# Optimization experiments

Hardware: AMD Instinct MI355X
Metric: run time of the kernel (lower is better)

## Reference

```python
import jax, jax.numpy as jnp
import numpy as np

N = 20000      # nodes
E = 320000     # edges (avg degree 16)
F_IN = 32      # raw node feature dim
D = 128        # GNN_EMBEDDING_DIM = out_channels per head
HEADS = 4
RNN_H = 128    # RNN_HIDDEN_DIM
NEG_SLOPE = 0.2


def setup_inputs() -> dict:
    key = jax.random.key(0)
    ks = jax.random.split(key, 16)
    s = 0.05
    return {
        "node_features": jax.random.normal(ks[0], (N, F_IN), jnp.float32),
        "hidden_state": jax.random.normal(ks[1], (1, RNN_H), jnp.float32),
        "W_enc": jax.random.normal(ks[2], (F_IN, D), jnp.float32) * s,
        "b_enc": jax.random.normal(ks[3], (D,), jnp.float32) * s,
        "W_l": jax.random.normal(ks[4], (D, HEADS * D), jnp.float32) * s,
        "b_l": jax.random.normal(ks[5], (HEADS * D,), jnp.float32) * s,
        "W_r": jax.random.normal(ks[6], (D, HEADS * D), jnp.float32) * s,
        "b_r": jax.random.normal(ks[7], (HEADS * D,), jnp.float32) * s,
        "att": jax.random.normal(ks[8], (HEADS, D), jnp.float32) * s,
        "gat_bias": jax.random.normal(ks[9], (D,), jnp.float32) * s,
        "W_ih": jax.random.normal(ks[10], (3 * RNN_H, D), jnp.float32) * s,
        "W_hh": jax.random.normal(ks[11], (3 * RNN_H, RNN_H), jnp.float32) * s,
        "b_ih": jax.random.normal(ks[12], (3 * RNN_H,), jnp.float32) * s,
        "b_hh": jax.random.normal(ks[13], (3 * RNN_H,), jnp.float32) * s,
        "edge_index": jax.random.randint(ks[14], (2, E), 0, N, jnp.int32),
    }


def reference(node_features, hidden_state, W_enc, b_enc, W_l, b_l, W_r, b_r,
              att, gat_bias, W_ih, W_hh, b_ih, b_hh, edge_index):
    n = node_features.shape[0]
    # node encoder + ReLU
    h = jax.nn.relu(node_features @ W_enc + b_enc)                 # [N, D]

    # GATv2Conv (heads=4, concat=False), add_self_loops=True, eval (no dropout)
    loop = jnp.arange(n, dtype=edge_index.dtype)
    src = jnp.concatenate([edge_index[0], loop])                   # source j
    dst = jnp.concatenate([edge_index[1], loop])                   # target i

    xl = (h @ W_l + b_l).reshape(n, HEADS, D)                      # source proj
    xr = (h @ W_r + b_r).reshape(n, HEADS, D)                      # target proj

    e = jax.nn.leaky_relu(xl[src] + xr[dst], NEG_SLOPE)            # [Et, H, C]
    logits = jnp.einsum('ehc,hc->eh', e, att)                      # [Et, H]

    # segment softmax over incoming edges of each target node
    m = jax.ops.segment_max(logits, dst, num_segments=n)           # [N, H]
    m = jnp.where(jnp.isfinite(m), m, 0.0)
    p = jnp.exp(logits - m[dst])
    denom = jax.ops.segment_sum(p, dst, num_segments=n)
    alpha = p / jnp.maximum(denom[dst], 1e-16)                     # [Et, H]

    out = jax.ops.segment_sum(xl[src] * alpha[..., None], dst, num_segments=n)
    gat = out.mean(axis=1) + gat_bias                              # [N, D]

    # agent node 0 -> GRUCell (torch gate order: r, z, n)
    x = gat[0:1]                                                   # [1, D]
    gi = x @ W_ih.T + b_ih
    gh = hidden_state @ W_hh.T + b_hh
    i_r, i_z, i_n = jnp.split(gi, 3, axis=-1)
    h_r, h_z, h_n = jnp.split(gh, 3, axis=-1)
    r = jax.nn.sigmoid(i_r + h_r)
    z = jax.nn.sigmoid(i_z + h_z)
    ng = jnp.tanh(i_n + r * h_n)
    return (1.0 - z) * ng + z * hidden_state                       # [1, RNN_H]
```

## Files before the change

kernel.cpp:

```cpp
#include <hip/hip_runtime.h>


#define NXL2 32
#define NSC  96
#define NBLK (NXL2 + NSC)
#define SLOTS 8
#define CAP  40
#define FLAGMAGIC 0x5A5A0000u

#define WEo  0
#define WLo  4096
#define WRo  6144
#define WIo  8192
#define WHo  9728
#define NFo  11264
#define HSo  12544
#define XL2o 17664
#define LGLo 18304
#define ALPo 19584
#define BUFSZ 19744

#define A_LG  0
#define A_XRP 64
#define A_XR  128
#define A_HP  160
#define A_GB  288
#define A_GAT 416
#define A_GH  544
#define A_GI  556
#define A_BI  568
#define A_BH  580

struct KP {
    const int* ei; int E;
    const float *nf, *W_enc, *b_enc, *W_l, *b_l, *W_r, *b_r, *att, *gat_bias,
                *hprev, *W_ih, *W_hh, *b_ih, *b_hh;
    unsigned *scnt;
    unsigned *xlflag;
    unsigned *o0flag;
    int      *sslots;
    float *lgpart;
    float *out0;
    float *out;
};

__device__ __forceinline__ unsigned pollFlag(unsigned* p) {
    for (long it = 0; it < 50000000L; ++it) {
        unsigned v = atomicOr(p, 0u);
        if ((v & 0xFFFF0000u) == FLAGMAGIC) return v & 0xFFFFu;
        __builtin_amdgcn_s_sleep(2);
    }
    return 0u;
}

__device__ __forceinline__ float sigm(float x) { return 1.f / (1.f + expf(-x)); }

__global__ __launch_bounds__(256) void k_all(KP p)
{
    __shared__ __align__(16) float buf[BUFSZ];
    __shared__ float aux[640];
    __shared__ int   iaux[128];
    const int t = threadIdx.x, b = blockIdx.x;

    if (b >= NXL2) {
        int s = b - NXL2;
        if (t == 0) iaux[0] = 0;
        __syncthreads();
        if ((p.E & 3) == 0) {
            int nv = p.E >> 2;
            int per = (nv + NSC - 1) / NSC;
            int lo = s * per, hi = min(lo + per, nv);
            const int4* d4 = (const int4*)(p.ei + p.E);
            for (int base = lo; base < hi; base += 1024) {
                int4 v[4];
                #pragma unroll
                for (int k = 0; k < 4; ++k) {
                    int i = base + t + k * 256;
                    v[k] = (i < hi) ? d4[i] : make_int4(1, 1, 1, 1);
                }
                #pragma unroll
                for (int k = 0; k < 4; ++k) {
                    int i = base + t + k * 256;
                    if (v[k].x == 0 || v[k].y == 0 || v[k].z == 0 || v[k].w == 0) {
                        #pragma unroll
                        for (int c = 0; c < 4; ++c) {
                            if ((&v[k].x)[c] == 0) {
                                int q = atomicAdd(&iaux[0], 1);
                                if (q < SLOTS) iaux[8 + q] = p.ei[4 * (long)i + c];
                            }
                        }
                    }
                }
            }
        } else {
            int per = (p.E + NSC - 1) / NSC;
            long lo = (long)s * per, hi = lo + per; if (hi > p.E) hi = p.E;
            for (long i = lo + t; i < hi; i += 256) {
                if (p.ei[p.E + i] == 0) {
                    int q = atomicAdd(&iaux[0], 1);
                    if (q < SLOTS) iaux[8 + q] = p.ei[i];
                }
            }
        }
        __syncthreads();
        int myc = min(iaux[0], SLOTS);
        if (t < myc) p.sslots[s * SLOTS + t] = iaux[8 + t];
        __syncthreads();
        __threadfence();
        if (t == 0) atomicExch(&p.scnt[s * 16], FLAGMAGIC | (unsigned)myc);
        return;
    }

    const int l4 = t & 15, g16 = t >> 4;
    const int j = b * 16 + l4;

    float blv = p.b_l[j], atv = p.att[j];
    float brv = (t < 16) ? p.b_r[b * 16 + t] : 0.f;
    if (t < 128) { aux[A_HP + t] = p.hprev[t]; aux[A_GB + t] = p.gat_bias[t]; }
    if (t >= 128 && t < 140) {
        int rr = t - 128, gate = rr >> 2, rin = rr & 3;
        aux[A_BI + rr] = p.b_ih[gate * 128 + b * 4 + rin];
        aux[A_BH + rr] = p.b_hh[gate * 128 + b * 4 + rin];
    }

    for (int idx = t; idx < 1024; idx += 256)
        ((float4*)(buf + WEo))[idx] = ((const float4*)p.W_enc)[idx];
    for (int idx = t; idx < 512; idx += 256) {
        int row = idx >> 2, f4 = idx & 3;
        ((float4*)(buf + WLo))[idx] = *(const float4*)(p.W_l + (long)row * 512 + b * 16 + f4 * 4);
    }
    for (int idx = t; idx < 512; idx += 256) {
        int row = idx >> 2, f4 = idx & 3;
        ((float4*)(buf + WRo))[idx] = *(const float4*)(p.W_r + (long)row * 512 + b * 16 + f4 * 4);
    }
    for (int idx = t; idx < 384; idx += 256) {
        int rr = idx >> 5, f4 = idx & 31;
        int grow = (rr >> 2) * 128 + b * 4 + (rr & 3);
        ((float4*)(buf + WIo))[idx] = *(const float4*)(p.W_ih + (long)grow * 128 + f4 * 4);
    }
    for (int idx = t; idx < 384; idx += 256) {
        int rr = idx >> 5, f4 = idx & 31;
        int grow = (rr >> 2) * 128 + b * 4 + (rr & 3);
        ((float4*)(buf + WHo))[idx] = *(const float4*)(p.W_hh + (long)grow * 128 + f4 * 4);
    }

    if (t < NSC) iaux[32 + t] = (int)pollFlag(&p.scnt[t * 16]);
    __syncthreads();
    __threadfence();
    if (t < 64) {
        int s0 = 2 * t, s1 = 2 * t + 1;
        int c0 = (s0 < NSC) ? iaux[32 + s0] : 0;
        int c1 = (s1 < NSC) ? iaux[32 + s1] : 0;
        int sum = c0 + c1, pre = sum;
        #pragma unroll
        for (int off = 1; off < 64; off <<= 1) {
            int v = __shfl_up(pre, off);
            if (t >= off) pre += v;
        }
        int base = pre - sum;
        for (int u = 0; u < c0; ++u) { if (base < CAP - 1) iaux[64 + base] = p.sslots[s0 * SLOTS + u]; ++base; }
        for (int u = 0; u < c1; ++u) { if (base < CAP - 1) iaux[64 + base] = p.sslots[s1 * SLOTS + u]; ++base; }
        if (t == 63) iaux[1] = min(pre, CAP - 1);
    }
    __syncthreads();
    int Mc = iaux[1];
    if (t == 0) iaux[64 + Mc] = 0;
    __syncthreads();
    int Mt = Mc + 1;

    for (int idx = t; idx < Mt * 8; idx += 256) {
        int e = idx >> 3, f4 = idx & 7;
        ((float4*)(buf + NFo))[idx] = *(const float4*)(p.nf + (long)iaux[64 + e] * 32 + f4 * 4);
    }
    __syncthreads();
    {
        int eg = t >> 7, c = t & 127;
        for (int e = eg; e < Mt; e += 2) {
            float a0 = 0, a1 = 0, a2 = 0, a3 = 0;
            #pragma unroll
            for (int k = 0; k < 32; k += 4) {
                a0 += buf[NFo + e * 32 + k]     * buf[WEo + k * 128 + c];
                a1 += buf[NFo + e * 32 + k + 1] * buf[WEo + (k + 1) * 128 + c];
                a2 += buf[NFo + e * 32 + k + 2] * buf[WEo + (k + 2) * 128 + c];
                a3 += buf[NFo + e * 32 + k + 3] * buf[WEo + (k + 3) * 128 + c];
            }
            buf[HSo + e * 128 + c] = fmaxf(a0 + a1 + a2 + a3 + p.b_enc[c], 0.f);
        }
    }
    __syncthreads();
    if (t < 64) {
        int col = t & 15, ch = t >> 4;
        const float* h0 = &buf[HSo + (Mt - 1) * 128];
        float s = 0.f;
        #pragma unroll 8
        for (int cc = 0; cc < 32; ++cc) {
            int c = ch * 32 + cc;
            s += h0[c] * buf[WRo + c * 16 + col];
        }
        aux[A_XRP + t] = s;
    }
    int ne = 0, el[3] = {0, 0, 0};
    for (int e = g16; e < Mt; e += 16) el[ne++] = e;
    float acc[3] = {0, 0, 0};
    #pragma unroll 4
    for (int c = 0; c < 128; c += 4) {
        float w0 = buf[WLo + c * 16 + l4],       w1 = buf[WLo + (c + 1) * 16 + l4];
        float w2 = buf[WLo + (c + 2) * 16 + l4], w3 = buf[WLo + (c + 3) * 16 + l4];
        #pragma unroll
        for (int k = 0; k < 3; ++k) {
            if (k < ne) {
                float4 h4 = *(const float4*)&buf[HSo + el[k] * 128 + c];
                acc[k] += h4.x * w0 + h4.y * w1 + h4.z * w2 + h4.w * w3;
            }
        }
    }
    __syncthreads();
    if (t < 16) aux[A_XR + t] = aux[A_XRP + t] + aux[A_XRP + 16 + t]
                              + aux[A_XRP + 32 + t] + aux[A_XRP + 48 + t] + brv;
    __syncthreads();
    {
        float xrj = aux[A_XR + l4];
        #pragma unroll
        for (int k = 0; k < 3; ++k) {
            if (k < ne) {
                int e = el[k];
                float xv = acc[k] + blv;
                buf[XL2o + e * 16 + l4] = xv;
                float v = xv + xrj;
                v = (v > 0.f) ? v : 0.2f * v;
                float pp = v * atv;
                #pragma unroll
                for (int off = 8; off; off >>= 1) pp += __shfl_down(pp, off, 16);
                if (l4 == 0) aux[A_LG + e] = pp;
            }
        }
    }
    __syncthreads();
    if (t < Mt) p.lgpart[b * CAP + t] = aux[A_LG + t];
    __syncthreads();
    __threadfence();
    if (t == 0) atomicExch(&p.xlflag[b * 16], FLAGMAGIC | 1u);

    {
        int w = t >> 6, l = t & 63;
        #pragma unroll
        for (int i = 0; i < 3; ++i) {
            int rr = w * 3 + i;
            float2 wv = ((const float2*)&buf[WHo + rr * 128])[l];
            float pp = wv.x * aux[A_HP + 2 * l] + wv.y * aux[A_HP + 2 * l + 1];
            #pragma unroll
            for (int off = 32; off; off >>= 1) pp += __shfl_down(pp, off);
            if (l == 0) aux[A_GH + rr] = pp + aux[A_BH + rr];
        }
    }

    if (t < NXL2) pollFlag(&p.xlflag[t * 16]);
    __syncthreads();
    __threadfence();
    for (int idx = t; idx < NXL2 * CAP; idx += 256)
        buf[LGLo + idx] = p.lgpart[idx];
    __syncthreads();
    if (t < 4) {
        int h = t;
        float m = -1e30f;
        for (int e = 0; e < Mt; ++e) {
            float lv = 0.f;
            #pragma unroll
            for (int q = 0; q < 8; ++q) lv += buf[LGLo + (8 * h + q) * CAP + e];
            buf[ALPo + e * 4 + h] = lv;
            m = fmaxf(m, lv);
        }
        float d = 0.f;
        for (int e = 0; e < Mt; ++e) d += expf(buf[ALPo + e * 4 + h] - m);
        float inv = 1.f / fmaxf(d, 1e-16f);
        for (int e = 0; e < Mt; ++e)
            buf[ALPo + e * 4 + h] = expf(buf[ALPo + e * 4 + h] - m) * inv;
    }
    __syncthreads();
    if (t < 16) {
        int h = b >> 3;
        float s = 0.f;
        for (int e = 0; e < Mt; ++e)
            s += buf[ALPo + e * 4 + h] * buf[XL2o + e * 16 + t];
        p.out0[b * 16 + t] = s;
    }
    __syncthreads();
    __threadfence();
    if (t == 0) atomicExch(&p.o0flag[b * 16], FLAGMAGIC | 1u);

    if (t < NXL2) pollFlag(&p.o0flag[t * 16]);
    __syncthreads();
    __threadfence();
    if (t < 128)
        aux[A_GAT + t] = 0.25f * (p.out0[t] + p.out0[128 + t] +
                                  p.out0[256 + t] + p.out0[384 + t]) + aux[A_GB + t];
    __syncthreads();
    {
        int w = t >> 6, l = t & 63;
        #pragma unroll
        for (int i = 0; i < 3; ++i) {
            int rr = w * 3 + i;
            float2 wv = ((const float2*)&buf[WIo + rr * 128])[l];
            float pp = wv.x * aux[A_GAT + 2 * l] + wv.y * aux[A_GAT + 2 * l + 1];
            #pragma unroll
            for (int off = 32; off; off >>= 1) pp += __shfl_down(pp, off);
            if (l == 0) aux[A_GI + rr] = pp + aux[A_BI + rr];
        }
    }
    __syncthreads();
    if (t < 4) {
        int c = b * 4 + t;
        float r = sigm(aux[A_GI + t]     + aux[A_GH + t]);
        float z = sigm(aux[A_GI + 4 + t] + aux[A_GH + 4 + t]);
        float n = tanhf(aux[A_GI + 8 + t] + r * aux[A_GH + 8 + t]);
        p.out[c] = (1.f - z) * n + z * aux[A_HP + c];
    }
}

extern "C" void kernel_launch(void* const* d_in, const int* in_sizes, int n_in,
                              void* d_out, int out_size, void* d_ws, size_t ws_size,
                              hipStream_t stream) {
    KP kp;
    kp.nf       = (const float*)d_in[0];
    kp.hprev    = (const float*)d_in[1];
    kp.W_enc    = (const float*)d_in[2];
    kp.b_enc    = (const float*)d_in[3];
    kp.W_l      = (const float*)d_in[4];
    kp.b_l      = (const float*)d_in[5];
    kp.W_r      = (const float*)d_in[6];
    kp.b_r      = (const float*)d_in[7];
    kp.att      = (const float*)d_in[8];
    kp.gat_bias = (const float*)d_in[9];
    kp.W_ih     = (const float*)d_in[10];
    kp.W_hh     = (const float*)d_in[11];
    kp.b_ih     = (const float*)d_in[12];
    kp.b_hh     = (const float*)d_in[13];
    kp.ei       = (const int*)d_in[14];
    kp.E = in_sizes[14] / 2;

    char* ws = (char*)d_ws;
    kp.scnt   = (unsigned*)(ws + 0);
    kp.xlflag = (unsigned*)(ws + 6144);
    kp.o0flag = (unsigned*)(ws + 8192);
    kp.sslots = (int*)(ws + 10240);
    kp.lgpart = (float*)(ws + 13312);
    kp.out0   = (float*)(ws + 18432);
    kp.out    = (float*)d_out;

    k_all<<<NBLK, 256, 0, stream>>>(kp);
}
```

Before: 118.0 us.

## Move encoder to scanner blocks and drop second grid-wide barrier

Scanner blocks now compute the encoder ReLU output for the source nodes they find and publish those rows, so worker blocks no longer gather raw features and re-encode them after the barrier. The GRU hidden-side matvec, the input-bias-independent gi precompute and the node-0 target projection are moved ahead of the scanner poll, so they overlap the wait. Each worker publishes its full xl slice, and every block then reduces all four heads redundantly, which removes the second flag-based grid barrier (o0flag). The poll loop also drops its sleep, spinning more aggressively, and uses a larger workspace.

```diff
diff --git a/kernel.cpp b/kernel.cpp
--- a/kernel.cpp
+++ b/kernel.cpp
@@ -1,9 +1,9 @@
 #include <hip/hip_runtime.h>
 
 
-#define NXL2 32
-#define NSC  96
-#define NBLK (NXL2 + NSC)
+#define NW   32
+#define NS   96
+#define NBLK (NW + NS)
 #define SLOTS 8
 #define CAP  40
 #define FLAGMAGIC 0x5A5A0000u
@@ -11,25 +11,26 @@
 #define WEo  0
 #define WLo  4096
 #define WRo  6144
-#define WIo  8192
-#define WHo  9728
-#define NFo  11264
-#define HSo  12544
-#define XL2o 17664
-#define LGLo 18304
-#define ALPo 19584
-#define BUFSZ 19744
-
-#define A_LG  0
-#define A_XRP 64
+#define HSo  8192
+#define XLo  0
+#define LGLo 20480
+#define ALPo 21760
+#define WIo  21920
+#define WHo  23456
+#define BUFSZ 24992
+
+#define A_H0  0
 #define A_XR  128
-#define A_HP  160
-#define A_GB  288
-#define A_GAT 416
-#define A_GH  544
-#define A_GI  556
-#define A_BI  568
-#define A_BH  580
+#define A_XRP 144
+#define A_HP  208
+#define A_GH  336
+#define A_GIB 348
+#define A_GAT 360
+#define A_LGP 488
+#define A_NF0 528
+#define A_BI  560
+#define A_BHH 572
+#define AUXSZ 584
 
 struct KP {
     const int* ei; int E;
@@ -37,18 +38,16 @@
                 *hprev, *W_ih, *W_hh, *b_ih, *b_hh;
     unsigned *scnt;
     unsigned *xlflag;
-    unsigned *o0flag;
-    int      *sslots;
+    float *hsslot;
     float *lgpart;
-    float *out0;
+    float *xlpub;
     float *out;
 };
 
 __device__ __forceinline__ unsigned pollFlag(unsigned* p) {
-    for (long it = 0; it < 50000000L; ++it) {
+    for (long it = 0; it < 20000000L; ++it) {
         unsigned v = atomicOr(p, 0u);
         if ((v & 0xFFFF0000u) == FLAGMAGIC) return v & 0xFFFFu;
-        __builtin_amdgcn_s_sleep(2);
     }
     return 0u;
 }
@@ -58,17 +57,17 @@
 __global__ __launch_bounds__(256) void k_all(KP p)
 {
     __shared__ __align__(16) float buf[BUFSZ];
-    __shared__ float aux[640];
-    __shared__ int   iaux[128];
+    __shared__ __align__(16) float aux[AUXSZ];
+    __shared__ int iaux[208];
     const int t = threadIdx.x, b = blockIdx.x;
 
-    if (b >= NXL2) {
-        int s = b - NXL2;
+    if (b >= NW) {
+        int s = b - NW;
         if (t == 0) iaux[0] = 0;
         __syncthreads();
         if ((p.E & 3) == 0) {
             int nv = p.E >> 2;
-            int per = (nv + NSC - 1) / NSC;
+            int per = (nv + NS - 1) / NS;
             int lo = s * per, hi = min(lo + per, nv);
             const int4* d4 = (const int4*)(p.ei + p.E);
             for (int base = lo; base < hi; base += 1024) {
@@ -93,7 +92,7 @@
                 }
             }
         } else {
-            int per = (p.E + NSC - 1) / NSC;
+            int per = (p.E + NS - 1) / NS;
             long lo = (long)s * per, hi = lo + per; if (hi > p.E) hi = p.E;
             for (long i = lo + t; i < hi; i += 256) {
                 if (p.ei[p.E + i] == 0) {
@@ -102,9 +101,34 @@
                 }
             }
         }
+        for (int idx = t; idx < 1024; idx += 256)
+            ((float4*)(buf + WEo))[idx] = ((const float4*)p.W_enc)[idx];
+        float bev = (t < 128) ? p.b_enc[t] : 0.f;
         __syncthreads();
         int myc = min(iaux[0], SLOTS);
-        if (t < myc) p.sslots[s * SLOTS + t] = iaux[8 + t];
+        if (myc > 0) {
+            for (int idx = t; idx < myc * 8; idx += 256) {
+                int e = idx >> 3, f4 = idx & 7;
+                ((float4*)aux)[e * 8 + f4] =
+                    *(const float4*)(p.nf + (long)iaux[8 + e] * 32 + f4 * 4);
+            }
+            __syncthreads();
+            for (int e = 0; e < myc; ++e) {
+                if (t < 128) {
+                    const float* x = aux + e * 32;
+                    float a0 = 0, a1 = 0, a2 = 0, a3 = 0;
+                    #pragma unroll
+                    for (int k = 0; k < 32; k += 4) {
+                        a0 += x[k]     * buf[WEo + k * 128 + t];
+                        a1 += x[k + 1] * buf[WEo + (k + 1) * 128 + t];
+                        a2 += x[k + 2] * buf[WEo + (k + 2) * 128 + t];
+                        a3 += x[k + 3] * buf[WEo + (k + 3) * 128 + t];
+                    }
+                    p.hsslot[(long)(s * SLOTS + e) * 128 + t] =
+                        fmaxf(a0 + a1 + a2 + a3 + bev, 0.f);
+                }
+            }
+        }
         __syncthreads();
         __threadfence();
         if (t == 0) atomicExch(&p.scnt[s * 16], FLAGMAGIC | (unsigned)myc);
@@ -115,90 +139,112 @@
     const int j = b * 16 + l4;
 
     float blv = p.b_l[j], atv = p.att[j];
+    float bev = (t < 128) ? p.b_enc[t] : 0.f;
     float brv = (t < 16) ? p.b_r[b * 16 + t] : 0.f;
-    if (t < 128) { aux[A_HP + t] = p.hprev[t]; aux[A_GB + t] = p.gat_bias[t]; }
+    if (t < 128) { aux[A_HP + t] = p.hprev[t]; aux[A_GAT + t] = p.gat_bias[t]; }
     if (t >= 128 && t < 140) {
-        int rr = t - 128, gate = rr >> 2, rin = rr & 3;
-        aux[A_BI + rr] = p.b_ih[gate * 128 + b * 4 + rin];
-        aux[A_BH + rr] = p.b_hh[gate * 128 + b * 4 + rin];
-    }
+        int rr = t - 128;
+        int grow = (rr >> 2) * 128 + b * 4 + (rr & 3);
+        aux[A_BI + rr] = p.b_ih[grow];
+        aux[A_BHH + rr] = p.b_hh[grow];
+    }
+    if (t >= 192 && t < 224) aux[A_NF0 + (t - 192)] = p.nf[t - 192];
 
     for (int idx = t; idx < 1024; idx += 256)
         ((float4*)(buf + WEo))[idx] = ((const float4*)p.W_enc)[idx];
     for (int idx = t; idx < 512; idx += 256) {
         int row = idx >> 2, f4 = idx & 3;
         ((float4*)(buf + WLo))[idx] = *(const float4*)(p.W_l + (long)row * 512 + b * 16 + f4 * 4);
-    }
-    for (int idx = t; idx < 512; idx += 256) {
-        int row = idx >> 2, f4 = idx & 3;
         ((float4*)(buf + WRo))[idx] = *(const float4*)(p.W_r + (long)row * 512 + b * 16 + f4 * 4);
     }
     for (int idx = t; idx < 384; idx += 256) {
         int rr = idx >> 5, f4 = idx & 31;
         int grow = (rr >> 2) * 128 + b * 4 + (rr & 3);
         ((float4*)(buf + WIo))[idx] = *(const float4*)(p.W_ih + (long)grow * 128 + f4 * 4);
-    }
-    for (int idx = t; idx < 384; idx += 256) {
-        int rr = idx >> 5, f4 = idx & 31;
-        int grow = (rr >> 2) * 128 + b * 4 + (rr & 3);
         ((float4*)(buf + WHo))[idx] = *(const float4*)(p.W_hh + (long)grow * 128 + f4 * 4);
     }
-
-    if (t < NSC) iaux[32 + t] = (int)pollFlag(&p.scnt[t * 16]);
-    __syncthreads();
-    __threadfence();
-    if (t < 64) {
-        int s0 = 2 * t, s1 = 2 * t + 1;
-        int c0 = (s0 < NSC) ? iaux[32 + s0] : 0;
-        int c1 = (s1 < NSC) ? iaux[32 + s1] : 0;
-        int sum = c0 + c1, pre = sum;
-        #pragma unroll
-        for (int off = 1; off < 64; off <<= 1) {
-            int v = __shfl_up(pre, off);
-            if (t >= off) pre += v;
-        }
-        int base = pre - sum;
-        for (int u = 0; u < c0; ++u) { if (base < CAP - 1) iaux[64 + base] = p.sslots[s0 * SLOTS + u]; ++base; }
-        for (int u = 0; u < c1; ++u) { if (base < CAP - 1) iaux[64 + base] = p.sslots[s1 * SLOTS + u]; ++base; }
-        if (t == 63) iaux[1] = min(pre, CAP - 1);
-    }
-    __syncthreads();
-    int Mc = iaux[1];
-    if (t == 0) iaux[64 + Mc] = 0;
-    __syncthreads();
-    int Mt = Mc + 1;
-
-    for (int idx = t; idx < Mt * 8; idx += 256) {
-        int e = idx >> 3, f4 = idx & 7;
-        ((float4*)(buf + NFo))[idx] = *(const float4*)(p.nf + (long)iaux[64 + e] * 32 + f4 * 4);
-    }
-    __syncthreads();
-    {
-        int eg = t >> 7, c = t & 127;
-        for (int e = eg; e < Mt; e += 2) {
-            float a0 = 0, a1 = 0, a2 = 0, a3 = 0;
-            #pragma unroll
-            for (int k = 0; k < 32; k += 4) {
-                a0 += buf[NFo + e * 32 + k]     * buf[WEo + k * 128 + c];
-                a1 += buf[NFo + e * 32 + k + 1] * buf[WEo + (k + 1) * 128 + c];
-                a2 += buf[NFo + e * 32 + k + 2] * buf[WEo + (k + 2) * 128 + c];
-                a3 += buf[NFo + e * 32 + k + 3] * buf[WEo + (k + 3) * 128 + c];
-            }
-            buf[HSo + e * 128 + c] = fmaxf(a0 + a1 + a2 + a3 + p.b_enc[c], 0.f);
-        }
+    __syncthreads();
+
+    if (t < 128) {
+        float a0 = 0, a1 = 0, a2 = 0, a3 = 0;
+        #pragma unroll
+        for (int k = 0; k < 32; k += 4) {
+            a0 += aux[A_NF0 + k]     * buf[WEo + k * 128 + t];
+            a1 += aux[A_NF0 + k + 1] * buf[WEo + (k + 1) * 128 + t];
+            a2 += aux[A_NF0 + k + 2] * buf[WEo + (k + 2) * 128 + t];
+            a3 += aux[A_NF0 + k + 3] * buf[WEo + (k + 3) * 128 + t];
+        }
+        aux[A_H0 + t] = fmaxf(a0 + a1 + a2 + a3 + bev, 0.f);
     }
     __syncthreads();
     if (t < 64) {
         int col = t & 15, ch = t >> 4;
-        const float* h0 = &buf[HSo + (Mt - 1) * 128];
         float s = 0.f;
         #pragma unroll 8
         for (int cc = 0; cc < 32; ++cc) {
             int c = ch * 32 + cc;
-            s += h0[c] * buf[WRo + c * 16 + col];
+            s += aux[A_H0 + c] * buf[WRo + c * 16 + col];
         }
         aux[A_XRP + t] = s;
     }
+    __syncthreads();
+    if (t < 16) aux[A_XR + t] = aux[A_XRP + t] + aux[A_XRP + 16 + t]
+                              + aux[A_XRP + 32 + t] + aux[A_XRP + 48 + t] + brv;
+    {
+        int w = t >> 6, l = t & 63;
+        #pragma unroll
+        for (int i = 0; i < 3; ++i) {
+            int rr = w * 3 + i;
+            float2 wv = ((const float2*)&buf[WHo + rr * 128])[l];
+            float pp = wv.x * aux[A_HP + 2 * l] + wv.y * aux[A_HP + 2 * l + 1];
+            #pragma unroll
+            for (int off = 32; off; off >>= 1) pp += __shfl_down(pp, off);
+            if (l == 0) aux[A_GH + rr] = pp + aux[A_BHH + rr];
+        }
+    }
+    {
+        int w = t >> 6, l = t & 63;
+        #pragma unroll
+        for (int i = 0; i < 3; ++i) {
+            int rr = w * 3 + i;
+            float2 wv = ((const float2*)&buf[WIo + rr * 128])[l];
+            float pp = wv.x * aux[A_GAT + 2 * l] + wv.y * aux[A_GAT + 2 * l + 1];
+            #pragma unroll
+            for (int off = 32; off; off >>= 1) pp += __shfl_down(pp, off);
+            if (l == 0) aux[A_GIB + rr] = pp + aux[A_BI + rr];
+        }
+    }
+
+    if (t < NS) iaux[t] = (int)pollFlag(&p.scnt[t * 16]);
+    __syncthreads();
+    __threadfence();
+    if (t < 64) {
+        int s0 = 2 * t, s1 = 2 * t + 1;
+        int c0 = (s0 < NS) ? iaux[s0] : 0;
+        int c1 = (s1 < NS) ? iaux[s1] : 0;
+        int sum = c0 + c1, pre = sum;
+        #pragma unroll
+        for (int off = 1; off < 64; off <<= 1) {
+            int v = __shfl_up(pre, off);
+            if (t >= off) pre += v;
+        }
+        int base = pre - sum;
+        for (int u = 0; u < c0; ++u) { if (base < CAP - 1) iaux[104 + base] = s0 * SLOTS + u; ++base; }
+        for (int u = 0; u < c1; ++u) { if (base < CAP - 1) iaux[104 + base] = s1 * SLOTS + u; ++base; }
+        if (t == 63) iaux[100] = min(pre, CAP - 1);
+    }
+    __syncthreads();
+    int Mc = iaux[100];
+    int Mt = Mc + 1;
+
+    for (int idx = t; idx < Mc * 32; idx += 256) {
+        int e = idx >> 5, f4 = idx & 31;
+        ((float4*)(buf + HSo))[e * 32 + f4] =
+            *(const float4*)(p.hsslot + (long)iaux[104 + e] * 128 + f4 * 4);
+    }
+    if (t < 128) buf[HSo + Mc * 128 + t] = aux[A_H0 + t];
+    __syncthreads();
+
     int ne = 0, el[3] = {0, 0, 0};
     for (int e = g16; e < Mt; e += 16) el[ne++] = e;
     float acc[3] = {0, 0, 0};
@@ -214,10 +260,6 @@
             }
         }
     }
-    __syncthreads();
-    if (t < 16) aux[A_XR + t] = aux[A_XRP + t] + aux[A_XRP + 16 + t]
-                              + aux[A_XRP + 32 + t] + aux[A_XRP + 48 + t] + brv;
-    __syncthreads();
     {
         float xrj = aux[A_XR + l4];
         #pragma unroll
@@ -225,40 +267,29 @@
             if (k < ne) {
                 int e = el[k];
                 float xv = acc[k] + blv;
-                buf[XL2o + e * 16 + l4] = xv;
+                p.xlpub[(long)e * 512 + j] = xv;
                 float v = xv + xrj;
                 v = (v > 0.f) ? v : 0.2f * v;
                 float pp = v * atv;
                 #pragma unroll
                 for (int off = 8; off; off >>= 1) pp += __shfl_down(pp, off, 16);
-                if (l4 == 0) aux[A_LG + e] = pp;
-            }
-        }
-    }
-    __syncthreads();
-    if (t < Mt) p.lgpart[b * CAP + t] = aux[A_LG + t];
+                if (l4 == 0) aux[A_LGP + e] = pp;
+            }
+        }
+    }
+    __syncthreads();
+    if (t < Mt) p.lgpart[b * CAP + t] = aux[A_LGP + t];
     __syncthreads();
     __threadfence();
     if (t == 0) atomicExch(&p.xlflag[b * 16], FLAGMAGIC | 1u);
 
-    {
-        int w = t >> 6, l = t & 63;
-        #pragma unroll
-        for (int i = 0; i < 3; ++i) {
-            int rr = w * 3 + i;
-            float2 wv = ((const float2*)&buf[WHo + rr * 128])[l];
-            float pp = wv.x * aux[A_HP + 2 * l] + wv.y * aux[A_HP + 2 * l + 1];
-            #pragma unroll
-            for (int off = 32; off; off >>= 1) pp += __shfl_down(pp, off);
-            if (l == 0) aux[A_GH + rr] = pp + aux[A_BH + rr];
-        }
-    }
-
-    if (t < NXL2) pollFlag(&p.xlflag[t * 16]);
+    if (t < NW) pollFlag(&p.xlflag[t * 16]);
     __syncthreads();
     __threadfence();
-    for (int idx = t; idx < NXL2 * CAP; idx += 256)
-        buf[LGLo + idx] = p.lgpart[idx];
+    for (int idx = t; idx < Mt * 128; idx += 256)
+        ((float4*)(buf + XLo))[idx] = ((const float4*)p.xlpub)[idx];
+    for (int idx = t; idx < 320; idx += 256)
+        ((float4*)(buf + LGLo))[idx] = ((const float4*)p.lgpart)[idx];
     __syncthreads();
     if (t < 4) {
         int h = t;
@@ -277,23 +308,18 @@
             buf[ALPo + e * 4 + h] = expf(buf[ALPo + e * 4 + h] - m) * inv;
     }
     __syncthreads();
-    if (t < 16) {
-        int h = b >> 3;
-        float s = 0.f;
-        for (int e = 0; e < Mt; ++e)
-            s += buf[ALPo + e * 4 + h] * buf[XL2o + e * 16 + t];
-        p.out0[b * 16 + t] = s;
-    }
-    __syncthreads();
-    __threadfence();
-    if (t == 0) atomicExch(&p.o0flag[b * 16], FLAGMAGIC | 1u);
-
-    if (t < NXL2) pollFlag(&p.o0flag[t * 16]);
-    __syncthreads();
-    __threadfence();
-    if (t < 128)
-        aux[A_GAT + t] = 0.25f * (p.out0[t] + p.out0[128 + t] +
-                                  p.out0[256 + t] + p.out0[384 + t]) + aux[A_GB + t];
+    if (t < 128) {
+        float s0 = 0, s1 = 0, s2 = 0, s3 = 0;
+        for (int e = 0; e < Mt; ++e) {
+            const float* al = &buf[ALPo + e * 4];
+            const float* xr = &buf[XLo + e * 512];
+            s0 += al[0] * xr[t];
+            s1 += al[1] * xr[128 + t];
+            s2 += al[2] * xr[256 + t];
+            s3 += al[3] * xr[384 + t];
+        }
+        aux[A_GAT + t] = 0.25f * (s0 + s1 + s2 + s3);
+    }
     __syncthreads();
     {
         int w = t >> 6, l = t & 63;
@@ -304,15 +330,15 @@
             float pp = wv.x * aux[A_GAT + 2 * l] + wv.y * aux[A_GAT + 2 * l + 1];
             #pragma unroll
             for (int off = 32; off; off >>= 1) pp += __shfl_down(pp, off);
-            if (l == 0) aux[A_GI + rr] = pp + aux[A_BI + rr];
+            if (l == 0) aux[A_XRP + rr] = pp + aux[A_GIB + rr];
         }
     }
     __syncthreads();
     if (t < 4) {
         int c = b * 4 + t;
-        float r = sigm(aux[A_GI + t]     + aux[A_GH + t]);
-        float z = sigm(aux[A_GI + 4 + t] + aux[A_GH + 4 + t]);
-        float n = tanhf(aux[A_GI + 8 + t] + r * aux[A_GH + 8 + t]);
+        float r = sigm(aux[A_XRP + t]     + aux[A_GH + t]);
+        float z = sigm(aux[A_XRP + 4 + t] + aux[A_GH + 4 + t]);
+        float n = tanhf(aux[A_XRP + 8 + t] + r * aux[A_GH + 8 + t]);
         p.out[c] = (1.f - z) * n + z * aux[A_HP + c];
     }
 }
@@ -341,10 +367,9 @@
     char* ws = (char*)d_ws;
     kp.scnt   = (unsigned*)(ws + 0);
     kp.xlflag = (unsigned*)(ws + 6144);
-    kp.o0flag = (unsigned*)(ws + 8192);
-    kp.sslots = (int*)(ws + 10240);
-    kp.lgpart = (float*)(ws + 13312);
-    kp.out0   = (float*)(ws + 18432);
+    kp.hsslot = (float*)(ws + 8192);
+    kp.lgpart = (float*)(ws + 401408);
+    kp.xlpub  = (float*)(ws + 406528);
     kp.out    = (float*)d_out;
 
     k_all<<<NBLK, 256, 0, stream>>>(kp);
```

Measured after the change: 109.7 us. -7.0%, faster.
